# Kernel tuning notes

Hardware: AMD Instinct MI355X
Metric: run time of the kernel (lower is better)

The kernel has to match this reference:

```python
import jax, jax.numpy as jnp
import numpy as np

# Mamba2 config derived from __init__ defaults
D_MODEL, D_STATE, D_CONV, EXPAND, HEADDIM = 768, 16, 4, 2, 64
D_INNER = EXPAND * D_MODEL                      # 1536
NHEADS = D_INNER // HEADDIM                     # 24
NGROUPS = 1
CONV_DIM = D_INNER + 2 * NGROUPS * D_STATE      # 1568
D_IN_PROJ = 2 * D_INNER + 2 * NGROUPS * D_STATE + NHEADS  # 3128
EPS = 1e-5


def setup_inputs() -> dict:
    key = jax.random.key(0)
    ks = jax.random.split(key, 8)
    B, L = 2, 4096
    x = jax.random.normal(ks[0], (B, L, D_MODEL), jnp.float32)
    s_in = 1.0 / np.sqrt(D_MODEL)
    s_out = 1.0 / np.sqrt(D_INNER)
    W_in = jax.random.uniform(ks[1], (D_IN_PROJ, D_MODEL), jnp.float32, -s_in, s_in)
    W_out = jax.random.uniform(ks[2], (D_MODEL, D_INNER), jnp.float32, -s_out, s_out)
    conv_w = jax.random.uniform(ks[3], (CONV_DIM, D_CONV), jnp.float32, -0.5, 0.5)
    conv_b = jax.random.uniform(ks[4], (CONV_DIM,), jnp.float32, -0.5, 0.5)
    # dt init in [1e-3, 0.1] (log-uniform), stored as inverse-softplus bias
    dt = jnp.exp(jax.random.uniform(ks[5], (NHEADS,), jnp.float32) * (np.log(0.1) - np.log(1e-3)) + np.log(1e-3))
    dt_bias = dt + jnp.log(-jnp.expm1(-dt))
    A_log = jnp.log(jax.random.uniform(ks[6], (NHEADS,), jnp.float32, 1.0, 16.0))
    D = jnp.ones((NHEADS,), jnp.float32)
    ln_w = jnp.ones((D_MODEL,), jnp.float32)
    ln_b = jnp.zeros((D_MODEL,), jnp.float32)
    gate_norm_w = jnp.ones((D_INNER,), jnp.float32)
    return dict(x=x, ln_w=ln_w, ln_b=ln_b, W_in=W_in, conv_w=conv_w, conv_b=conv_b,
                dt_bias=dt_bias, A_log=A_log, D=D, gate_norm_w=gate_norm_w, W_out=W_out)


def _layernorm(x, w, b):
    mu = x.mean(-1, keepdims=True)
    var = ((x - mu) ** 2).mean(-1, keepdims=True)
    return (x - mu) * jax.lax.rsqrt(var + EPS) * w + b


def _silu(x):
    return x * jax.nn.sigmoid(x)


def _mamba_block(x, ln_w, ln_b, W_in, conv_w, conv_b, dt_bias, A_log, D, gate_norm_w, W_out):
    Bsz, L, _ = x.shape
    u = _layernorm(x, ln_w, ln_b)
    zxbcdt = jnp.einsum('bld,ed->ble', u, W_in)                 # (b,l,3128)
    z = zxbcdt[..., :D_INNER]
    xBC = zxbcdt[..., D_INNER:D_INNER + CONV_DIM]
    dt = jax.nn.softplus(zxbcdt[..., -NHEADS:] + dt_bias)       # (b,l,h)
    # causal depthwise conv (width D_CONV) + SiLU
    xp = jnp.pad(xBC, ((0, 0), (D_CONV - 1, 0), (0, 0)))
    acc = xp[:, 0:L, :] * conv_w[:, 0]
    for i in range(1, D_CONV):
        acc = acc + xp[:, i:i + L, :] * conv_w[:, i]
    xBC = _silu(acc + conv_b)
    xs = xBC[..., :D_INNER].reshape(Bsz, L, NHEADS, HEADDIM)    # (b,l,h,p)
    Bm = xBC[..., D_INNER:D_INNER + D_STATE]                    # (b,l,n) ngroups=1
    Cm = xBC[..., D_INNER + D_STATE:]                           # (b,l,n)
    A = -jnp.exp(A_log)                                         # (h,)
    dA = jnp.exp(dt * A)                                        # (b,l,h)
    # selective scan: h_t = dA_t * h_{t-1} + dt_t * (x_t outer B_t)
    def step(h, inp):
        dA_t, dt_t, B_t, C_t, x_t = inp                          # (b,h),(b,h),(b,n),(b,n),(b,h,p)
        h = dA_t[..., None, None] * h + jnp.einsum('bh,bn,bhp->bhpn', dt_t, B_t, x_t)
        y = jnp.einsum('bhpn,bn->bhp', h, C_t)
        return h, y
    h0 = jnp.zeros((Bsz, NHEADS, HEADDIM, D_STATE), x.dtype)
    _, ys = jax.lax.scan(step, h0, (dA.transpose(1, 0, 2), dt.transpose(1, 0, 2),
                                    Bm.transpose(1, 0, 2), Cm.transpose(1, 0, 2),
                                    xs.transpose(1, 0, 2, 3)))
    y = ys.transpose(1, 0, 2, 3) + D[:, None] * xs               # (b,l,h,p) skip term
    y = y.reshape(Bsz, L, D_INNER)
    # gated RMSNorm: norm(y * silu(z)) * weight
    g = y * _silu(z)
    g = g * jax.lax.rsqrt((g * g).mean(-1, keepdims=True) + EPS) * gate_norm_w
    out = jnp.einsum('ble,de->bld', g, W_out)
    return x + out


def reference(x, ln_w, ln_b, W_in, conv_w, conv_b, dt_bias, A_log, D, gate_norm_w, W_out):
    return _mamba_block(x, ln_w, ln_b, W_in, conv_w, conv_b, dt_bias, A_log, D, gate_norm_w, W_out)
```

## Files before the change

kernel.cpp:

```cpp
#include <hip/hip_runtime.h>
#include <hip/hip_bf16.h>
#include <stdint.h>

#define SEQ      4096
#define BATCH    2
#define NTOK     (BATCH*SEQ)
#define DMODEL   768
#define DINNER   1536
#define NHEADS   24
#define HEADDIM  64
#define DSTATE   16
#define NPAD     3200
#define EPSV     1e-5f
#define CHUNK    64
#define NCHUNK   (SEQ/CHUNK)
#define SUB      32

typedef __bf16 bf16x8 __attribute__((ext_vector_type(8)));
typedef float  floatx4 __attribute__((ext_vector_type(4)));

__device__ __forceinline__ unsigned short f2bf(float f) {
    union { float f; uint32_t u; } v; v.f = f;
    uint32_t u = v.u;
    uint32_t r = (u + 0x7fffu + ((u >> 16) & 1u)) >> 16;
    return (unsigned short)r;
}

__device__ __forceinline__ float bf2f(unsigned short h) {
    union { uint32_t u; float f; } v; v.u = (uint32_t)h << 16;
    return v.f;
}

__device__ __forceinline__ float bfl(uint32_t u) {
    union { uint32_t u; float f; } v; v.u = u << 16; return v.f;
}
__device__ __forceinline__ float bfh(uint32_t u) {
    union { uint32_t u; float f; } v; v.u = u & 0xffff0000u; return v.f;
}
__device__ __forceinline__ uint32_t packbf(float lo, float hi) {
    return (uint32_t)f2bf(lo) | ((uint32_t)f2bf(hi) << 16);
}

__device__ __forceinline__ float siluf(float x) { return x / (1.f + __expf(-x)); }

__device__ __forceinline__ void async_cp16(const void* g, void* l) {
    __builtin_amdgcn_global_load_lds(
        (const __attribute__((address_space(1))) void*)g,
        (__attribute__((address_space(3))) void*)l,
        16, 0, 0);
}

__global__ __launch_bounds__(256) void cvt_kernel(
    const float* __restrict__ Win, const float* __restrict__ Wout,
    unsigned short* __restrict__ win16, unsigned short* __restrict__ wout16)
{
    int idx = blockIdx.x * 256 + threadIdx.x;
    const int n1 = NPAD * DMODEL;
    if (idx < n1) {
        int r = idx / DMODEL;
        win16[idx] = (r < 3128) ? f2bf(Win[idx]) : (unsigned short)0;
    } else {
        int i2 = idx - n1;
        if (i2 < DMODEL * DINNER) wout16[i2] = f2bf(Wout[i2]);
    }
}

__global__ __launch_bounds__(256) void ln_kernel(
    const float* __restrict__ x, const float* __restrict__ lnw, const float* __restrict__ lnb,
    unsigned short* __restrict__ u16)
{
    int wave = threadIdx.x >> 6, lane = threadIdx.x & 63;
    int token = blockIdx.x * 4 + wave;
    const float* row = x + (size_t)token * DMODEL;
    float4 v[3];
    float s = 0.f, ss = 0.f;
#pragma unroll
    for (int j = 0; j < 3; ++j) {
        v[j] = *(const float4*)(row + lane*4 + j*256);
        s  += v[j].x + v[j].y + v[j].z + v[j].w;
        ss += v[j].x*v[j].x + v[j].y*v[j].y + v[j].z*v[j].z + v[j].w*v[j].w;
    }
#pragma unroll
    for (int o = 32; o > 0; o >>= 1) { s += __shfl_xor(s, o, 64); ss += __shfl_xor(ss, o, 64); }
    float mean = s * (1.f/768.f);
    float var  = ss * (1.f/768.f) - mean*mean;
    float rstd = rsqrtf(var + EPSV);
    unsigned short* brow = u16 + (size_t)token * DMODEL;
#pragma unroll
    for (int j = 0; j < 3; ++j) {
        int cidx = lane*4 + j*256;
        float4 w4 = *(const float4*)(lnw + cidx);
        float4 b4 = *(const float4*)(lnb + cidx);
        float a0 = (v[j].x - mean)*rstd*w4.x + b4.x;
        float a1 = (v[j].y - mean)*rstd*w4.y + b4.y;
        float a2 = (v[j].z - mean)*rstd*w4.z + b4.z;
        float a3 = (v[j].w - mean)*rstd*w4.w + b4.w;
        ushort4 p; p.x = f2bf(a0); p.y = f2bf(a1); p.z = f2bf(a2); p.w = f2bf(a3);
        *(ushort4*)(brow + cidx) = p;
    }
}

__global__ __launch_bounds__(256) void dt_kernel(
    const float* __restrict__ raw24, const float* __restrict__ dt_bias,
    const float* __restrict__ A_log, float* __restrict__ dtT, float* __restrict__ dAT)
{
    int tid = blockIdx.x * 256 + threadIdx.x;
    int h   = tid >> 13;
    int tok = tid & (NTOK-1);
    float raw = raw24[(size_t)tok*NHEADS + h] + dt_bias[h];
    float dt = (raw > 20.f) ? raw : log1pf(__expf(raw));
    float A = -__expf(A_log[h]);
    dtT[tid] = dt;
    dAT[tid] = __expf(dt * A);
}

__global__ __launch_bounds__(256, 3) void gemm1_kernel(
    const unsigned short* __restrict__ A, const unsigned short* __restrict__ Bt,
    unsigned short* __restrict__ z16, unsigned short* __restrict__ x16,
    float* __restrict__ bcr, float* __restrict__ raw24)
{
    constexpr int K = DMODEL;
    __shared__ unsigned short As[128*64];
    __shared__ unsigned short Bs[128*64];
    const int tid  = threadIdx.x;
    const int lane = tid & 63;
    const int wave = tid >> 6;
    const int id   = blockIdx.x;
    const int xcd  = id & 7;
    const int j5   = id >> 3;
    const int m0 = (xcd*8 + (j5 & 7)) * 128;
    const int n0 = (j5 >> 3) * 128;
    const int wm = (wave & 1) * 64;
    const int wn = (wave >> 1) * 64;

    floatx4 acc[4][4];
#pragma unroll
    for (int i = 0; i < 4; ++i)
#pragma unroll
        for (int j = 0; j < 4; ++j) acc[i][j] = floatx4{0.f, 0.f, 0.f, 0.f};

    const int srow8  = lane >> 3;
    const int schunk = lane & 7;
    const int sscol  = (schunk ^ srow8) * 8;

    for (int k0 = 0; k0 < K; k0 += 64) {
        __syncthreads();
#pragma unroll
        for (int o = 0; o < 4; ++o) {
            int row = wave*32 + o*8 + srow8;
            async_cp16(A + (size_t)(m0 + row) * K + k0 + sscol, As + row*64 + schunk*8);
        }
#pragma unroll
        for (int o = 0; o < 4; ++o) {
            int row = wave*32 + o*8 + srow8;
            async_cp16(Bt + (size_t)(n0 + row) * K + k0 + sscol, Bs + row*64 + schunk*8);
        }
        __syncthreads();
        const int fr  = lane & 15;
        const int q8  = lane >> 4;
        const int key = fr & 7;
#pragma unroll
        for (int ks = 0; ks < 2; ++ks) {
            const int ch = ((ks*4 + q8) ^ key) * 8;
            bf16x8 a[4], b[4];
#pragma unroll
            for (int i = 0; i < 4; ++i)
                a[i] = *(const bf16x8*)(As + (wm + i*16 + fr)*64 + ch);
#pragma unroll
            for (int j = 0; j < 4; ++j)
                b[j] = *(const bf16x8*)(Bs + (wn + j*16 + fr)*64 + ch);
#pragma unroll
            for (int i = 0; i < 4; ++i)
#pragma unroll
                for (int j = 0; j < 4; ++j)
                    acc[i][j] = __builtin_amdgcn_mfma_f32_16x16x32_bf16(a[i], b[j], acc[i][j], 0, 0, 0);
        }
    }

    const int col = lane & 15;
    const int rq  = (lane >> 4) * 4;
    if (n0 < DINNER) {
#pragma unroll
        for (int i = 0; i < 4; ++i)
#pragma unroll
            for (int j = 0; j < 4; ++j)
#pragma unroll
                for (int r = 0; r < 4; ++r) {
                    int gm = m0 + wm + i*16 + rq + r;
                    int gn = n0 + wn + j*16 + col;
                    z16[(size_t)gm * DINNER + gn] = f2bf(acc[i][j][r]);
                }
    } else if (n0 < 3072) {
#pragma unroll
        for (int i = 0; i < 4; ++i)
#pragma unroll
            for (int j = 0; j < 4; ++j)
#pragma unroll
                for (int r = 0; r < 4; ++r) {
                    int gm = m0 + wm + i*16 + rq + r;
                    int gn = n0 + wn + j*16 + col;
                    x16[(size_t)gm * DINNER + (gn - DINNER)] = f2bf(acc[i][j][r]);
                }
    } else {
#pragma unroll
        for (int i = 0; i < 4; ++i)
#pragma unroll
            for (int j = 0; j < 4; ++j)
#pragma unroll
                for (int r = 0; r < 4; ++r) {
                    int gm = m0 + wm + i*16 + rq + r;
                    int gn = n0 + wn + j*16 + col;
                    if (gn < 3104)
                        bcr[(size_t)gm * 32 + (gn - 3072)] = acc[i][j][r];
                    else if (gn < 3128)
                        raw24[(size_t)gm * NHEADS + (gn - 3104)] = acc[i][j][r];
                }
    }
}

__global__ __launch_bounds__(256, 4) void gemm2_kernel(
    const unsigned short* __restrict__ A, const unsigned short* __restrict__ Bt,
    float* __restrict__ Cf, const float* __restrict__ resid)
{
    constexpr int K = DINNER;
    __shared__ unsigned short As[64*64];
    __shared__ unsigned short Bs[128*64];
    const int tid  = threadIdx.x;
    const int lane = tid & 63;
    const int wave = tid >> 6;
    const int id   = blockIdx.x;
    const int xcd  = id & 7;
    const int j6   = id >> 3;
    const int m0 = (xcd*16 + j6/6) * 64;
    const int n0 = (j6 % 6) * 128;
    const int wm = (wave & 1) * 32;
    const int wn = (wave >> 1) * 64;

    floatx4 acc[2][4];
#pragma unroll
    for (int i = 0; i < 2; ++i)
#pragma unroll
        for (int j = 0; j < 4; ++j) acc[i][j] = floatx4{0.f, 0.f, 0.f, 0.f};

    const int srow8  = lane >> 3;
    const int schunk = lane & 7;
    const int sscol  = (schunk ^ srow8) * 8;

    for (int k0 = 0; k0 < K; k0 += 64) {
        __syncthreads();
#pragma unroll
        for (int o = 0; o < 2; ++o) {
            int row = wave*16 + o*8 + srow8;
            async_cp16(A + (size_t)(m0 + row) * K + k0 + sscol, As + row*64 + schunk*8);
        }
#pragma unroll
        for (int o = 0; o < 4; ++o) {
            int row = wave*32 + o*8 + srow8;
            async_cp16(Bt + (size_t)(n0 + row) * K + k0 + sscol, Bs + row*64 + schunk*8);
        }
        __syncthreads();
        const int fr  = lane & 15;
        const int q8  = lane >> 4;
        const int key = fr & 7;
#pragma unroll
        for (int ks = 0; ks < 2; ++ks) {
            const int ch = ((ks*4 + q8) ^ key) * 8;
            bf16x8 a[2], b[4];
#pragma unroll
            for (int i = 0; i < 2; ++i)
                a[i] = *(const bf16x8*)(As + (wm + i*16 + fr)*64 + ch);
#pragma unroll
            for (int j = 0; j < 4; ++j)
                b[j] = *(const bf16x8*)(Bs + (wn + j*16 + fr)*64 + ch);
#pragma unroll
            for (int i = 0; i < 2; ++i)
#pragma unroll
                for (int j = 0; j < 4; ++j)
                    acc[i][j] = __builtin_amdgcn_mfma_f32_16x16x32_bf16(a[i], b[j], acc[i][j], 0, 0, 0);
        }
    }

    const int col = lane & 15;
    const int rq  = (lane >> 4) * 4;
#pragma unroll
    for (int i = 0; i < 2; ++i)
#pragma unroll
        for (int j = 0; j < 4; ++j)
#pragma unroll
            for (int r = 0; r < 4; ++r) {
                int gm = m0 + wm + i*16 + rq + r;
                int gn = n0 + wn + j*16 + col;
                Cf[(size_t)gm * DMODEL + gn] = acc[i][j][r] + resid[(size_t)gm * DMODEL + gn];
            }
}

__global__ __launch_bounds__(256) void scan_pass1(
    const unsigned short* __restrict__ x16, const float* __restrict__ bcr,
    const float* __restrict__ dAT, const float* __restrict__ dtT,
    const float* __restrict__ cw, const float* __restrict__ cb, const float* __restrict__ Dp,
    float* __restrict__ hloc, float* __restrict__ pprod, unsigned short* __restrict__ ylocal16)
{
    int wave = threadIdx.x >> 6, lane = threadIdx.x & 63;
    int blk = blockIdx.x * 4 + wave;
    int c = blk & (NCHUNK-1), bh = blk >> 6;
    int h = bh % NHEADS, b = bh / NHEADS;
    int row0 = b * SEQ + c * CHUNK;
    int l0 = c * CHUNK;
    int tb = h * NTOK + row0;
    __shared__ float bcraw[4][35][32];
    __shared__ float bcsc[4][32][32];
    __shared__ float av[4][32], dv[4][32];

    const int cx = h*64 + lane;
    float cwx0 = cw[cx*4+0], cwx1 = cw[cx*4+1], cwx2 = cw[cx*4+2], cwx3 = cw[cx*4+3];
    float cbx = cb[cx];
    const int nBC = lane & 31;
    float cwc0 = cw[(DINNER+nBC)*4+0], cwc1 = cw[(DINNER+nBC)*4+1];
    float cwc2 = cw[(DINNER+nBC)*4+2], cwc3 = cw[(DINNER+nBC)*4+3];
    float cbc = cb[DINNER+nBC];
    float Dh = Dp[h];

    float xm3 = (l0 >= 3) ? bf2f(x16[(size_t)(row0-3)*DINNER + cx]) : 0.f;
    float xm2 = (l0 >= 2) ? bf2f(x16[(size_t)(row0-2)*DINNER + cx]) : 0.f;
    float xm1 = (l0 >= 1) ? bf2f(x16[(size_t)(row0-1)*DINNER + cx]) : 0.f;

    float hst[16];
#pragma unroll
    for (int n = 0; n < 16; ++n) hst[n] = 0.f;
    float aprod = 1.f;

    for (int sc = 0; sc < CHUNK/SUB; ++sc) {
        int rb = row0 + sc * SUB;
        int lb = l0 + sc * SUB;
        __syncthreads();
#pragma unroll
        for (int it = 0; it < 5; ++it) {
            int idx = it*64 + lane;
            if (idx < 280) {
                int s = idx >> 3, q = idx & 7;
                float4 val = {0.f,0.f,0.f,0.f};
                if (lb - 3 + s >= 0)
                    val = *(const float4*)(bcr + (size_t)(rb-3+s)*32 + q*4);
                *(float4*)&bcraw[wave][s][q*4] = val;
            }
        }
        if (lane < 32) av[wave][lane] = dAT[(size_t)tb + sc*SUB + lane];
        else           dv[wave][lane-32] = dtT[(size_t)tb + sc*SUB + lane - 32];
        float xr[SUB];
#pragma unroll
        for (int s = 0; s < SUB; ++s)
            xr[s] = bf2f(x16[(size_t)(rb+s)*DINNER + cx]);
        __syncthreads();
#pragma unroll
        for (int it = 0; it < 16; ++it) {
            int s = it*2 + (lane >> 5);
            float v = cbc + bcraw[wave][s][nBC]*cwc0 + bcraw[wave][s+1][nBC]*cwc1
                          + bcraw[wave][s+2][nBC]*cwc2 + bcraw[wave][s+3][nBC]*cwc3;
            bcsc[wave][s][nBC] = siluf(v);
        }
        __syncthreads();
#pragma unroll 2
        for (int s = 0; s < SUB; ++s) {
            float a = av[wave][s];
            float xc = siluf(cbx + xm3*cwx0 + xm2*cwx1 + xm1*cwx2 + xr[s]*cwx3);
            xm3 = xm2; xm2 = xm1; xm1 = xr[s];
            float scale = dv[wave][s] * xc;
            float y = Dh * xc;
            const float4* bp4 = (const float4*)&bcsc[wave][s][0];
            float4 bv[8];
#pragma unroll
            for (int q = 0; q < 8; ++q) bv[q] = bp4[q];
            const float* bp = (const float*)bv;
#pragma unroll
            for (int n = 0; n < 16; ++n) hst[n] = a*hst[n] + scale*bp[n];
#pragma unroll
            for (int n = 0; n < 16; ++n) y += hst[n] * bp[16+n];
            aprod *= a;
            ylocal16[(size_t)(rb+s)*DINNER + cx] = f2bf(y);
        }
    }
    float* o = hloc + (size_t)blk * 1024 + lane * 16;
#pragma unroll
    for (int n = 0; n < 16; ++n) o[n] = hst[n];
    if (lane == 0) pprod[blk] = aprod;
}

__global__ __launch_bounds__(64) void scan_pass2(
    const float* __restrict__ hloc, const float* __restrict__ pprod, float* __restrict__ hstart)
{
    int bh = blockIdx.x, lane = threadIdx.x;
    float hst[16];
#pragma unroll
    for (int n = 0; n < 16; ++n) hst[n] = 0.f;
    for (int c = 0; c < NCHUNK; ++c) {
        int blk = bh * NCHUNK + c;
        float* o = hstart + (size_t)blk * 1024 + lane * 16;
#pragma unroll
        for (int n = 0; n < 16; ++n) o[n] = hst[n];
        float P = pprod[blk];
        const float* hl = hloc + (size_t)blk * 1024 + lane * 16;
#pragma unroll
        for (int n = 0; n < 16; ++n) hst[n] = P * hst[n] + hl[n];
    }
}

__global__ __launch_bounds__(256) void scan_pass3(
    const float* __restrict__ bcr, const float* __restrict__ dAT,
    const float* __restrict__ cw, const float* __restrict__ cb,
    const float* __restrict__ hstart, unsigned short* __restrict__ ylocal16)
{
    int wave = threadIdx.x >> 6, lane = threadIdx.x & 63;
    int blk = blockIdx.x * 4 + wave;
    int c = blk & (NCHUNK-1), bh = blk >> 6;
    int h = bh % NHEADS, b = bh / NHEADS;
    int row0 = b * SEQ + c * CHUNK;
    int l0 = c * CHUNK;
    int tb = h * NTOK + row0;
    __shared__ float craw[4][35][16];
    __shared__ float csc[4][32][16];
    __shared__ float av[4][32];

    const int cx = h*64 + lane;
    const int nC = lane & 15;
    float cwc0 = cw[(DINNER+16+nC)*4+0], cwc1 = cw[(DINNER+16+nC)*4+1];
    float cwc2 = cw[(DINNER+16+nC)*4+2], cwc3 = cw[(DINNER+16+nC)*4+3];
    float cbc = cb[DINNER+16+nC];

    float h0[16];
    const float* hs = hstart + (size_t)blk * 1024 + lane * 16;
#pragma unroll
    for (int n = 0; n < 16; ++n) h0[n] = hs[n];
    float cd = 1.f;

    for (int sc = 0; sc < CHUNK/SUB; ++sc) {
        int rb = row0 + sc * SUB;
        int lb = l0 + sc * SUB;
        __syncthreads();
#pragma unroll
        for (int it = 0; it < 3; ++it) {
            int idx = it*64 + lane;
            if (idx < 140) {
                int s = idx >> 2, q = idx & 3;
                float4 val = {0.f,0.f,0.f,0.f};
                if (lb - 3 + s >= 0)
                    val = *(const float4*)(bcr + (size_t)(rb-3+s)*32 + 16 + q*4);
                *(float4*)&craw[wave][s][q*4] = val;
            }
        }
        if (lane < 32) av[wave][lane] = dAT[(size_t)tb + sc*SUB + lane];
        float yr[SUB];
#pragma unroll
        for (int s = 0; s < SUB; ++s)
            yr[s] = bf2f(ylocal16[(size_t)(rb+s)*DINNER + cx]);
        __syncthreads();
#pragma unroll
        for (int it = 0; it < 8; ++it) {
            int s = it*4 + (lane >> 4);
            float v = cbc + craw[wave][s][nC]*cwc0 + craw[wave][s+1][nC]*cwc1
                          + craw[wave][s+2][nC]*cwc2 + craw[wave][s+3][nC]*cwc3;
            csc[wave][s][nC] = siluf(v);
        }
        __syncthreads();
#pragma unroll 2
        for (int s = 0; s < SUB; ++s) {
            cd *= av[wave][s];
            const float4* cp4 = (const float4*)&csc[wave][s][0];
            float4 cv[4];
#pragma unroll
            for (int q = 0; q < 4; ++q) cv[q] = cp4[q];
            const float* cp = (const float*)cv;
            float corr = 0.f;
#pragma unroll
            for (int n = 0; n < 16; ++n) corr += cp[n] * h0[n];
            ylocal16[(size_t)(rb+s)*DINNER + cx] = f2bf(yr[s] + cd * corr);
        }
    }
}

__global__ __launch_bounds__(256) void gate_kernel(
    const unsigned short* __restrict__ yv16, const unsigned short* __restrict__ z16,
    const float* __restrict__ gw, unsigned short* __restrict__ g16)
{
    int wave = threadIdx.x >> 6, lane = threadIdx.x & 63;
    int token = blockIdx.x * 4 + wave;
    const uint4* yrow = (const uint4*)(yv16 + (size_t)token * DINNER);
    const uint4* zrow = (const uint4*)(z16 + (size_t)token * DINNER);
    float g[3][8];
    float ss = 0.f;
#pragma unroll
    for (int j = 0; j < 3; ++j) {
        uint4 y8 = yrow[lane + j*64];
        uint4 z8 = zrow[lane + j*64];
        const uint32_t* yp = (const uint32_t*)&y8;
        const uint32_t* zp = (const uint32_t*)&z8;
#pragma unroll
        for (int q = 0; q < 4; ++q) {
            float a = bfl(yp[q]) * siluf(bfl(zp[q]));
            float bvl = bfh(yp[q]) * siluf(bfh(zp[q]));
            g[j][q*2]   = a;
            g[j][q*2+1] = bvl;
            ss += a*a + bvl*bvl;
        }
    }
#pragma unroll
    for (int o = 32; o > 0; o >>= 1) ss += __shfl_xor(ss, o, 64);
    float scale = rsqrtf(ss * (1.f/1536.f) + EPSV);
    uint4* orow = (uint4*)(g16 + (size_t)token * DINNER);
#pragma unroll
    for (int j = 0; j < 3; ++j) {
        int ebase = (lane + j*64) * 8;
        float4 w0 = *(const float4*)(gw + ebase);
        float4 w1 = *(const float4*)(gw + ebase + 4);
        uint4 p;
        p.x = packbf(g[j][0]*scale*w0.x, g[j][1]*scale*w0.y);
        p.y = packbf(g[j][2]*scale*w0.z, g[j][3]*scale*w0.w);
        p.z = packbf(g[j][4]*scale*w1.x, g[j][5]*scale*w1.y);
        p.w = packbf(g[j][6]*scale*w1.z, g[j][7]*scale*w1.w);
        orow[lane + j*64] = p;
    }
}

extern "C" void kernel_launch(void* const* d_in, const int* in_sizes, int n_in,
                              void* d_out, int out_size, void* d_ws, size_t ws_size,
                              hipStream_t stream)
{
    const float* x        = (const float*)d_in[0];
    const float* ln_w     = (const float*)d_in[1];
    const float* ln_b     = (const float*)d_in[2];
    const float* W_in     = (const float*)d_in[3];
    const float* conv_w   = (const float*)d_in[4];
    const float* conv_b   = (const float*)d_in[5];
    const float* dt_bias  = (const float*)d_in[6];
    const float* A_log    = (const float*)d_in[7];
    const float* Dp       = (const float*)d_in[8];
    const float* gate_w   = (const float*)d_in[9];
    const float* W_out    = (const float*)d_in[10];
    float* out = (float*)d_out;

    char* ws = (char*)d_ws;
    size_t off = 0;
    auto alloc = [&](size_t bytes) -> void* {
        void* p = ws + off;
        off += (bytes + 255) & ~(size_t)255;
        return p;
    };
    unsigned short* u16    = (unsigned short*)alloc((size_t)NTOK*DMODEL*2);
    unsigned short* win16  = (unsigned short*)alloc((size_t)NPAD*DMODEL*2);
    float*          dtT    = (float*)alloc((size_t)NTOK*NHEADS*4);
    float*          dAT    = (float*)alloc((size_t)NTOK*NHEADS*4);
    float*          raw24  = (float*)alloc((size_t)NTOK*NHEADS*4);
    unsigned short* x16    = (unsigned short*)alloc((size_t)NTOK*DINNER*2);
    float*          bcr    = (float*)alloc((size_t)NTOK*32*4);
    unsigned short* wout16 = (unsigned short*)alloc((size_t)DMODEL*DINNER*2);
    unsigned short* z16    = (unsigned short*)alloc((size_t)NTOK*DINNER*2);
    unsigned short* y16    = (unsigned short*)alloc((size_t)NTOK*DINNER*2);
    unsigned short* g16    = (unsigned short*)alloc((size_t)NTOK*DINNER*2);
    float*          pprod  = (float*)alloc((size_t)BATCH*NHEADS*NCHUNK*4);
    float* hloc   = (float*)u16;
    float* hstart = (float*)g16;

    cvt_kernel<<<(NPAD*DMODEL + DMODEL*DINNER)/256, 256, 0, stream>>>(W_in, W_out, win16, wout16);
    ln_kernel<<<NTOK/4, 256, 0, stream>>>(x, ln_w, ln_b, u16);
    gemm1_kernel<<<1600, 256, 0, stream>>>(u16, win16, z16, x16, bcr, raw24);
    dt_kernel<<<NTOK*NHEADS/256, 256, 0, stream>>>(raw24, dt_bias, A_log, dtT, dAT);
    scan_pass1<<<BATCH*NHEADS*NCHUNK/4, 256, 0, stream>>>(x16, bcr, dAT, dtT, conv_w, conv_b, Dp, hloc, pprod, y16);
    scan_pass2<<<BATCH*NHEADS, 64, 0, stream>>>(hloc, pprod, hstart);
    scan_pass3<<<BATCH*NHEADS*NCHUNK/4, 256, 0, stream>>>(bcr, dAT, conv_w, conv_b, hstart, y16);
    gate_kernel<<<NTOK/4, 256, 0, stream>>>(y16, z16, gate_w, g16);
    gemm2_kernel<<<768, 256, 0, stream>>>(g16, wout16, out, x);
}
```

Measured before the change: 278.8 us.

## Rewrite input-projection GEMM with 256x256 tiles and double-buffered async pipeline

The first GEMM now uses 512-thread blocks computing 256x256 output tiles. Its shared-memory A/B buffers are double-buffered and filled with async copies that are interleaved with MFMA phases under explicit barriers, waitcnts and s_setprio. NPAD grows to 3328 so the N dimension divides into 256-wide tiles, which adds some padded weight conversion and wasted compute. The aim is more data reuse per tile and overlap of global loads with matrix math, at the cost of larger register and LDS footprint and only 416 blocks.

```diff
diff --git a/kernel.cpp b/kernel.cpp
--- a/kernel.cpp
+++ b/kernel.cpp
@@ -10,11 +10,12 @@
 #define NHEADS   24
 #define HEADDIM  64
 #define DSTATE   16
-#define NPAD     3200
+#define NPAD     3328
 #define EPSV     1e-5f
 #define CHUNK    64
 #define NCHUNK   (SEQ/CHUNK)
 #define SUB      32
+#define NT       12
 
 typedef __bf16 bf16x8 __attribute__((ext_vector_type(8)));
 typedef float  floatx4 __attribute__((ext_vector_type(4)));
@@ -114,102 +115,193 @@
     dAT[tid] = __expf(dt * A);
 }
 
-__global__ __launch_bounds__(256, 3) void gemm1_kernel(
+__global__ __launch_bounds__(512, 2) void gemm1_kernel(
     const unsigned short* __restrict__ A, const unsigned short* __restrict__ Bt,
     unsigned short* __restrict__ z16, unsigned short* __restrict__ x16,
     float* __restrict__ bcr, float* __restrict__ raw24)
 {
-    constexpr int K = DMODEL;
-    __shared__ unsigned short As[128*64];
-    __shared__ unsigned short Bs[128*64];
+    __shared__ unsigned short As[2][256*64];
+    __shared__ unsigned short Bs[2][256*64];
     const int tid  = threadIdx.x;
     const int lane = tid & 63;
-    const int wave = tid >> 6;
-    const int id   = blockIdx.x;
-    const int xcd  = id & 7;
-    const int j5   = id >> 3;
-    const int m0 = (xcd*8 + (j5 & 7)) * 128;
-    const int n0 = (j5 >> 3) * 128;
-    const int wm = (wave & 1) * 64;
-    const int wn = (wave >> 1) * 64;
-
-    floatx4 acc[4][4];
-#pragma unroll
-    for (int i = 0; i < 4; ++i)
+    const int wid  = tid >> 6;
+    const int wr   = wid >> 2;
+    const int wc   = wid & 3;
+
+    const int id  = blockIdx.x;
+    const int xcd = id & 7;
+    const int jj  = id >> 3;
+    const int mt  = xcd * 4 + (jj & 3);
+    const int nt  = jj >> 2;
+    const int m0  = mt * 256;
+    const int n0  = nt * 256;
+
+    const int srow = tid >> 3;
+    const int sch  = tid & 7;
+    const int ssc  = (sch ^ (srow & 7)) * 8;
+
+    const unsigned short* Ag = A  + (size_t)(m0 + srow) * 768 + ssc;
+    const unsigned short* Bg = Bt + (size_t)(n0 + srow) * 768 + ssc;
+    unsigned short* AsD = &As[0][0] + srow * 64 + sch * 8;
+    unsigned short* BsD = &Bs[0][0] + srow * 64 + sch * 8;
+
+    auto stageA = [&](int bb, int ko) {
+        const unsigned short* g = Ag + ko;
+        unsigned short* d = AsD + bb * 16384;
+        async_cp16(g,            d);
+        async_cp16(g +  64*768,  d +  64*64);
+        async_cp16(g + 128*768,  d + 128*64);
+        async_cp16(g + 192*768,  d + 192*64);
+    };
+    auto stageB = [&](int bb, int h, int ko) {
+        const unsigned short* g = Bg + ko + (size_t)h * 128 * 768;
+        unsigned short* d = BsD + bb * 16384 + h * 128 * 64;
+        async_cp16(g,           d);
+        async_cp16(g + 64*768,  d + 64*64);
+    };
+
+    floatx4 acc[8][4];
+#pragma unroll
+    for (int i = 0; i < 8; ++i)
 #pragma unroll
         for (int j = 0; j < 4; ++j) acc[i][j] = floatx4{0.f, 0.f, 0.f, 0.f};
 
-    const int srow8  = lane >> 3;
-    const int schunk = lane & 7;
-    const int sscol  = (schunk ^ srow8) * 8;
-
-    for (int k0 = 0; k0 < K; k0 += 64) {
-        __syncthreads();
-#pragma unroll
-        for (int o = 0; o < 4; ++o) {
-            int row = wave*32 + o*8 + srow8;
-            async_cp16(A + (size_t)(m0 + row) * K + k0 + sscol, As + row*64 + schunk*8);
-        }
-#pragma unroll
-        for (int o = 0; o < 4; ++o) {
-            int row = wave*32 + o*8 + srow8;
-            async_cp16(Bt + (size_t)(n0 + row) * K + k0 + sscol, Bs + row*64 + schunk*8);
-        }
-        __syncthreads();
-        const int fr  = lane & 15;
-        const int q8  = lane >> 4;
-        const int key = fr & 7;
-#pragma unroll
-        for (int ks = 0; ks < 2; ++ks) {
-            const int ch = ((ks*4 + q8) ^ key) * 8;
-            bf16x8 a[4], b[4];
-#pragma unroll
-            for (int i = 0; i < 4; ++i)
-                a[i] = *(const bf16x8*)(As + (wm + i*16 + fr)*64 + ch);
+    const int fr  = lane & 15;
+    const int q8  = lane >> 4;
+    const int key = fr & 7;
+    const int ch0 = (q8 ^ key) * 8;
+    const int ch1 = ((4 + q8) ^ key) * 8;
+
+    stageA(0, 0);
+    stageB(0, 0, 0);
+    stageB(0, 1, 0);
+    stageA(1, 64);
+    asm volatile("s_waitcnt vmcnt(4)" ::: "memory");
+    __builtin_amdgcn_s_barrier();
+
+    for (int t = 0; t < NT; ++t) {
+        const int b = t & 1;
+        const unsigned short* ap = &As[0][0] + b * 16384 + (wr * 128 + fr) * 64;
+        const unsigned short* bp = &Bs[0][0] + b * 16384 + (wc * 64 + fr) * 64;
+        bf16x8 af[4][2], bf[4][2];
+
+#pragma unroll
+        for (int i = 0; i < 4; ++i) {
+            af[i][0] = *(const bf16x8*)(ap + i*1024 + ch0);
+            af[i][1] = *(const bf16x8*)(ap + i*1024 + ch1);
+        }
+#pragma unroll
+        for (int j = 0; j < 2; ++j) {
+            bf[j][0] = *(const bf16x8*)(bp + j*1024 + ch0);
+            bf[j][1] = *(const bf16x8*)(bp + j*1024 + ch1);
+        }
+        if (t + 1 < NT) stageB(b ^ 1, 0, (t + 1) * 64);
+        __builtin_amdgcn_s_barrier();
+        asm volatile("s_waitcnt lgkmcnt(0)");
+        __builtin_amdgcn_sched_barrier(0);
+        __builtin_amdgcn_s_setprio(1);
+#pragma unroll
+        for (int i = 0; i < 4; ++i)
+#pragma unroll
+            for (int j = 0; j < 2; ++j) {
+                acc[i][j] = __builtin_amdgcn_mfma_f32_16x16x32_bf16(af[i][0], bf[j][0], acc[i][j], 0, 0, 0);
+                acc[i][j] = __builtin_amdgcn_mfma_f32_16x16x32_bf16(af[i][1], bf[j][1], acc[i][j], 0, 0, 0);
+            }
+        __builtin_amdgcn_s_setprio(0);
+        __builtin_amdgcn_s_barrier();
+
+#pragma unroll
+        for (int j = 2; j < 4; ++j) {
+            bf[j][0] = *(const bf16x8*)(bp + j*1024 + ch0);
+            bf[j][1] = *(const bf16x8*)(bp + j*1024 + ch1);
+        }
+        if (t + 1 < NT) stageB(b ^ 1, 1, (t + 1) * 64);
+        __builtin_amdgcn_s_barrier();
+        asm volatile("s_waitcnt lgkmcnt(0)");
+        __builtin_amdgcn_sched_barrier(0);
+        __builtin_amdgcn_s_setprio(1);
+#pragma unroll
+        for (int i = 0; i < 4; ++i)
+#pragma unroll
+            for (int j = 2; j < 4; ++j) {
+                acc[i][j] = __builtin_amdgcn_mfma_f32_16x16x32_bf16(af[i][0], bf[j][0], acc[i][j], 0, 0, 0);
+                acc[i][j] = __builtin_amdgcn_mfma_f32_16x16x32_bf16(af[i][1], bf[j][1], acc[i][j], 0, 0, 0);
+            }
+        __builtin_amdgcn_s_setprio(0);
+        __builtin_amdgcn_s_barrier();
+
+#pragma unroll
+        for (int i = 0; i < 4; ++i) {
+            af[i][0] = *(const bf16x8*)(ap + (i + 4)*1024 + ch0);
+            af[i][1] = *(const bf16x8*)(ap + (i + 4)*1024 + ch1);
+        }
+        __builtin_amdgcn_s_barrier();
+        asm volatile("s_waitcnt lgkmcnt(0)");
+        __builtin_amdgcn_sched_barrier(0);
+        __builtin_amdgcn_s_setprio(1);
+#pragma unroll
+        for (int i = 0; i < 4; ++i)
+#pragma unroll
+            for (int j = 0; j < 2; ++j) {
+                acc[i+4][j] = __builtin_amdgcn_mfma_f32_16x16x32_bf16(af[i][0], bf[j][0], acc[i+4][j], 0, 0, 0);
+                acc[i+4][j] = __builtin_amdgcn_mfma_f32_16x16x32_bf16(af[i][1], bf[j][1], acc[i+4][j], 0, 0, 0);
+            }
+        __builtin_amdgcn_s_setprio(0);
+        __builtin_amdgcn_s_barrier();
+
+        if (t + 2 < NT) stageA(b, (t + 2) * 64);
+        __builtin_amdgcn_s_barrier();
+        asm volatile("s_waitcnt lgkmcnt(0)");
+        __builtin_amdgcn_sched_barrier(0);
+        __builtin_amdgcn_s_setprio(1);
+#pragma unroll
+        for (int i = 0; i < 4; ++i)
+#pragma unroll
+            for (int j = 2; j < 4; ++j) {
+                acc[i+4][j] = __builtin_amdgcn_mfma_f32_16x16x32_bf16(af[i][0], bf[j][0], acc[i+4][j], 0, 0, 0);
+                acc[i+4][j] = __builtin_amdgcn_mfma_f32_16x16x32_bf16(af[i][1], bf[j][1], acc[i+4][j], 0, 0, 0);
+            }
+        __builtin_amdgcn_s_setprio(0);
+        if (t + 2 < NT) { asm volatile("s_waitcnt vmcnt(4)" ::: "memory"); }
+        else            { asm volatile("s_waitcnt vmcnt(0)" ::: "memory"); }
+        __builtin_amdgcn_s_barrier();
+    }
+
+    const int colx = lane & 15;
+    const int rq   = (lane >> 4) * 4;
+    const int gmb  = m0 + wr * 128;
+    const int gnb  = n0 + wc * 64;
+    if (nt < 6) {
+#pragma unroll
+        for (int i = 0; i < 8; ++i)
 #pragma unroll
             for (int j = 0; j < 4; ++j)
-                b[j] = *(const bf16x8*)(Bs + (wn + j*16 + fr)*64 + ch);
-#pragma unroll
-            for (int i = 0; i < 4; ++i)
-#pragma unroll
-                for (int j = 0; j < 4; ++j)
-                    acc[i][j] = __builtin_amdgcn_mfma_f32_16x16x32_bf16(a[i], b[j], acc[i][j], 0, 0, 0);
-        }
-    }
-
-    const int col = lane & 15;
-    const int rq  = (lane >> 4) * 4;
-    if (n0 < DINNER) {
-#pragma unroll
-        for (int i = 0; i < 4; ++i)
-#pragma unroll
-            for (int j = 0; j < 4; ++j)
 #pragma unroll
                 for (int r = 0; r < 4; ++r) {
-                    int gm = m0 + wm + i*16 + rq + r;
-                    int gn = n0 + wn + j*16 + col;
+                    int gm = gmb + i*16 + rq + r;
+                    int gn = gnb + j*16 + colx;
                     z16[(size_t)gm * DINNER + gn] = f2bf(acc[i][j][r]);
                 }
-    } else if (n0 < 3072) {
-#pragma unroll
-        for (int i = 0; i < 4; ++i)
+    } else if (nt < 12) {
+#pragma unroll
+        for (int i = 0; i < 8; ++i)
 #pragma unroll
             for (int j = 0; j < 4; ++j)
 #pragma unroll
                 for (int r = 0; r < 4; ++r) {
-                    int gm = m0 + wm + i*16 + rq + r;
-                    int gn = n0 + wn + j*16 + col;
+                    int gm = gmb + i*16 + rq + r;
+                    int gn = gnb + j*16 + colx;
                     x16[(size_t)gm * DINNER + (gn - DINNER)] = f2bf(acc[i][j][r]);
                 }
     } else {
 #pragma unroll
-        for (int i = 0; i < 4; ++i)
+        for (int i = 0; i < 8; ++i)
 #pragma unroll
             for (int j = 0; j < 4; ++j)
 #pragma unroll
                 for (int r = 0; r < 4; ++r) {
-                    int gm = m0 + wm + i*16 + rq + r;
-                    int gn = n0 + wn + j*16 + col;
+                    int gm = gmb + i*16 + rq + r;
+                    int gn = gnb + j*16 + colx;
                     if (gn < 3104)
                         bcr[(size_t)gm * 32 + (gn - 3072)] = acc[i][j][r];
                     else if (gn < 3128)
@@ -561,7 +653,7 @@
 
     cvt_kernel<<<(NPAD*DMODEL + DMODEL*DINNER)/256, 256, 0, stream>>>(W_in, W_out, win16, wout16);
     ln_kernel<<<NTOK/4, 256, 0, stream>>>(x, ln_w, ln_b, u16);
-    gemm1_kernel<<<1600, 256, 0, stream>>>(u16, win16, z16, x16, bcr, raw24);
+    gemm1_kernel<<<416, 512, 0, stream>>>(u16, win16, z16, x16, bcr, raw24);
     dt_kernel<<<NTOK*NHEADS/256, 256, 0, stream>>>(raw24, dt_bias, A_log, dtT, dAT);
     scan_pass1<<<BATCH*NHEADS*NCHUNK/4, 256, 0, stream>>>(x16, bcr, dAT, dtT, conv_w, conv_b, Dp, hloc, pprod, y16);
     scan_pass2<<<BATCH*NHEADS, 64, 0, stream>>>(hloc, pprod, hstart);
```

New measurement: 286.1 us. 2.6% more time.

## Parallelize chunk-state propagation across four blocks per head with LDS staging

Applied to the files above, without the earlier changes.

The inter-chunk state propagation kernel previously ran one 64-thread block per batch-head, with each lane serially walking 64 chunks over 16 state elements with strided global loads. It now launches four 256-thread blocks per batch-head, each thread owning one state element. The kernel first bulk-loads all 64 chunks of its quarter into shared memory with coalesced float4 loads, then runs the serial recurrence from LDS with coalesced stores. This targets the tiny occupancy and uncoalesced access of the old kernel, at the cost of 64KB of shared memory per block.

```diff
diff --git a/kernel.cpp b/kernel.cpp
--- a/kernel.cpp
+++ b/kernel.cpp
@@ -385,22 +385,30 @@
     if (lane == 0) pprod[blk] = aprod;
 }
 
-__global__ __launch_bounds__(64) void scan_pass2(
+__global__ __launch_bounds__(256) void scan_pass2(
     const float* __restrict__ hloc, const float* __restrict__ pprod, float* __restrict__ hstart)
 {
-    int bh = blockIdx.x, lane = threadIdx.x;
-    float hst[16];
-#pragma unroll
-    for (int n = 0; n < 16; ++n) hst[n] = 0.f;
-    for (int c = 0; c < NCHUNK; ++c) {
-        int blk = bh * NCHUNK + c;
-        float* o = hstart + (size_t)blk * 1024 + lane * 16;
-#pragma unroll
-        for (int n = 0; n < 16; ++n) o[n] = hst[n];
-        float P = pprod[blk];
-        const float* hl = hloc + (size_t)blk * 1024 + lane * 16;
-#pragma unroll
-        for (int n = 0; n < 16; ++n) hst[n] = P * hst[n] + hl[n];
+    __shared__ float sm[64*256];
+    __shared__ float pp[64];
+    const int tid = threadIdx.x;
+    const int bh  = blockIdx.x >> 2;
+    const int q   = blockIdx.x & 3;
+    const float* src = hloc + (size_t)bh * 65536 + q * 256;
+#pragma unroll
+    for (int it = 0; it < 16; ++it) {
+        int idx = it*256 + tid;
+        int c   = idx >> 6;
+        int e4  = (idx & 63) * 4;
+        *(float4*)&sm[c*256 + e4] = *(const float4*)(src + (size_t)c*1024 + e4);
+    }
+    if (tid < 64) pp[tid] = pprod[bh*64 + tid];
+    __syncthreads();
+    float h = 0.f;
+    float* dst = hstart + (size_t)bh * 65536 + q * 256 + tid;
+#pragma unroll 8
+    for (int c = 0; c < 64; ++c) {
+        dst[(size_t)c * 1024] = h;
+        h = pp[c] * h + sm[c*256 + tid];
     }
 }
 
@@ -564,7 +572,7 @@
     gemm1_kernel<<<1600, 256, 0, stream>>>(u16, win16, z16, x16, bcr, raw24);
     dt_kernel<<<NTOK*NHEADS/256, 256, 0, stream>>>(raw24, dt_bias, A_log, dtT, dAT);
     scan_pass1<<<BATCH*NHEADS*NCHUNK/4, 256, 0, stream>>>(x16, bcr, dAT, dtT, conv_w, conv_b, Dp, hloc, pprod, y16);
-    scan_pass2<<<BATCH*NHEADS, 64, 0, stream>>>(hloc, pprod, hstart);
+    scan_pass2<<<BATCH*NHEADS*4, 256, 0, stream>>>(hloc, pprod, hstart);
     scan_pass3<<<BATCH*NHEADS*NCHUNK/4, 256, 0, stream>>>(bcr, dAT, conv_w, conv_b, hstart, y16);
     gate_kernel<<<NTOK/4, 256, 0, stream>>>(y16, z16, gate_w, g16);
     gemm2_kernel<<<768, 256, 0, stream>>>(g16, wout16, out, x);
```

Result: faster. 261.8 us (-6.1%).
